# Kernel optimization log

Hardware: AMD Instinct MI355X
Metric: run time of the kernel (lower is better)

## Reference

```python
import jax, jax.numpy as jnp
import numpy as np

N_NODES = 100000
N_EDGES = 1000000
N_GRAPHS = 1024
F_IN = 128
N_CLASSES = 10
BN_EPS = 1e-5


def _lin(key, fan_in, fan_out):
    k1, k2 = jax.random.split(key)
    b = 1.0 / np.sqrt(fan_in)
    W = jax.random.uniform(k1, (fan_out, fan_in), minval=-b, maxval=b, dtype=jnp.float32)
    bias = jax.random.uniform(k2, (fan_out,), minval=-b, maxval=b, dtype=jnp.float32)
    return W, bias


def setup_inputs() -> dict:
    key = jax.random.key(0)
    ks = jax.random.split(key, 16)
    inp = {
        "atom_feats": jax.random.normal(ks[0], (N_NODES, F_IN), dtype=jnp.float32),
        "edge_src": jax.random.randint(ks[1], (N_EDGES,), 0, N_NODES),
        "edge_dst": jax.random.randint(ks[2], (N_EDGES,), 0, N_NODES),
        "graph_ids": jnp.sort(jax.random.randint(ks[3], (N_NODES,), 0, N_GRAPHS)),
    }
    # conv1: F_IN -> 32 with batch-norm on edge features
    inp["Wt1"], inp["bt1"] = _lin(ks[4], F_IN, 32)
    inp["Wp1"], inp["bp1"] = _lin(ks[5], F_IN, 32)
    inp["bn_gamma"] = jnp.ones((32,), jnp.float32)
    inp["bn_beta"] = jnp.zeros((32,), jnp.float32)
    inp["bn_mean"] = jnp.zeros((32,), jnp.float32)
    inp["bn_var"] = jnp.ones((32,), jnp.float32)
    # conv2: 32 -> 64 ; conv3: 64 -> 64
    inp["Wt2"], inp["bt2"] = _lin(ks[6], 32, 64)
    inp["Wp2"], inp["bp2"] = _lin(ks[7], 32, 64)
    inp["Wt3"], inp["bt3"] = _lin(ks[8], 64, 64)
    inp["Wp3"], inp["bp3"] = _lin(ks[9], 64, 64)
    # fc layers
    inp["Wf1"], inp["bf1"] = _lin(ks[10], 64, 64)
    inp["Wf2"], inp["bf2"] = _lin(ks[11], 64, 32)
    inp["Wf3"], inp["bf3"] = _lin(ks[12], 32, N_CLASSES)
    return inp


def _seg_max(vals, ids, n):
    m = jax.ops.segment_max(vals, ids, num_segments=n)
    return jnp.where(jnp.isfinite(m), m, 0.0)  # zero-in-degree -> 0 (DGL semantics)


def _edgeconv(x, src, dst, Wt, bt, Wp, bp, bn=None):
    xs = x[src]                      # [E, f_in] gather src
    xd = x[dst]                      # [E, f_in] gather dst
    e = (xd - xs) @ Wt.T + bt + (xs @ Wp.T + bp)  # [E, f_out]
    if bn is not None:
        gamma, beta, mean, var = bn
        e = (e - mean) * (gamma / jnp.sqrt(var + BN_EPS)) + beta
    return _seg_max(e, dst, x.shape[0])


def reference(atom_feats, edge_src, edge_dst, graph_ids,
              Wt1, bt1, Wp1, bp1, bn_gamma, bn_beta, bn_mean, bn_var,
              Wt2, bt2, Wp2, bp2, Wt3, bt3, Wp3, bp3,
              Wf1, bf1, Wf2, bf2, Wf3, bf3):
    x = jax.nn.elu(_edgeconv(atom_feats, edge_src, edge_dst, Wt1, bt1, Wp1, bp1,
                             bn=(bn_gamma, bn_beta, bn_mean, bn_var)))
    x = jax.nn.elu(_edgeconv(x, edge_src, edge_dst, Wt2, bt2, Wp2, bp2))
    x = jax.nn.elu(_edgeconv(x, edge_src, edge_dst, Wt3, bt3, Wp3, bp3))
    x = _seg_max(x, graph_ids, N_GRAPHS)          # graph-level max pooling [G, 64]
    x = jax.nn.elu(x @ Wf1.T + bf1)               # dropout is identity in eval mode
    x = jax.nn.elu(x @ Wf2.T + bf2)
    x = x @ Wf3.T + bf3
    return jax.nn.log_softmax(x, axis=1)
```

## Files before the change

kernel.cpp:

```cpp
#include <hip/hip_runtime.h>
#include <hip/hip_fp16.h>
#include <math.h>

#define N_NODES 100000
#define N_EDGES 1000000
#define N_GRAPHS 1024
#define BN_EPS 1e-5f

#define BUCKET_NODES 128
#define NB_BUCKETS ((N_NODES + BUCKET_NODES - 1) / BUCKET_NODES)
#define BUCKET_PAD 2048
#define BUCKET_CAP 3072
#define SCAT_CHUNK 2048

typedef __attribute__((__ext_vector_type__(8))) _Float16 f16x8;
typedef __attribute__((__ext_vector_type__(4))) _Float16 f16x4;
typedef __attribute__((__ext_vector_type__(4))) float f32x4;

static __device__ __forceinline__ float elu_f(float v) {
    return v > 0.f ? v : expm1f(v);
}

static __device__ __forceinline__ unsigned pkmax(unsigned a, unsigned b) {
    unsigned r;
    asm("v_pk_max_f16 %0, %1, %2" : "=v"(r) : "v"(a), "v"(b));
    return r;
}
#define HALF2_NEG_INF 0xFC00FC00u

static __device__ __forceinline__ uint4 pkmax4(uint4 a, uint4 b) {
    uint4 r;
    r.x = pkmax(a.x, b.x);
    r.y = pkmax(a.y, b.y);
    r.z = pkmax(a.z, b.z);
    r.w = pkmax(a.w, b.w);
    return r;
}

static __device__ __forceinline__ unsigned fmap(float f) {
    unsigned u = __float_as_uint(f);
    return (u & 0x80000000u) ? ~u : (u | 0x80000000u);
}
static __device__ __forceinline__ float funmap(unsigned u) {
    unsigned b = (u & 0x80000000u) ? (u & 0x7FFFFFFFu) : ~u;
    return __uint_as_float(b);
}
#define NEG_INF_MAPPED 0x007FFFFFu

__global__ __launch_bounds__(256) void prep_kernel(
        const float* __restrict__ Wt1, const float* __restrict__ bt1,
        const float* __restrict__ Wp1, const float* __restrict__ bp1,
        const float* __restrict__ gamma, const float* __restrict__ beta,
        const float* __restrict__ mean,  const float* __restrict__ var,
        const float* __restrict__ Wt2, const float* __restrict__ bt2,
        const float* __restrict__ Wp2, const float* __restrict__ bp2,
        const float* __restrict__ Wt3, const float* __restrict__ bt3,
        const float* __restrict__ Wp3, const float* __restrict__ bp3,
        __half* __restrict__ wsz1, float* __restrict__ qb1,
        __half* __restrict__ wsz2, float* __restrict__ qb2,
        __half* __restrict__ wsz3, float* __restrict__ qb3,
        int* __restrict__ cursor, unsigned* __restrict__ pooled) {
    int idx = blockIdx.x * 256 + threadIdx.x;

    if (idx < NB_BUCKETS) cursor[idx] = 0;
    for (int j = idx; j < N_GRAPHS * 64; j += 8192) pooled[j] = NEG_INF_MAPPED;

    {
        const int K = 128, F = 32, NCF = 4;
        if (idx < K * 2 * F) {
            int frag = idx >> 9, within = idx & 511, lane = within >> 3, j = within & 7;
            int kf = frag / NCF, cf = frag % NCF;
            int k = kf * 32 + (lane >> 4) * 8 + j;
            int c = cf * 16 + (lane & 15);
            float v;
            if (c < F) {
                float s = gamma[c] * rsqrtf(var[c] + BN_EPS);
                v = Wt1[c * K + k] * s;
            } else {
                int cc = c - F;
                float s = gamma[cc] * rsqrtf(var[cc] + BN_EPS);
                v = (Wp1[cc * K + k] - Wt1[cc * K + k]) * s;
            }
            wsz1[idx] = __float2half(v);
        }
        if (idx < F) {
            float s = gamma[idx] * rsqrtf(var[idx] + BN_EPS);
            qb1[idx] = (bt1[idx] + bp1[idx]) * s + beta[idx] - mean[idx] * s;
        }
    }
    {
        const int K = 32, F = 64, NCF = 8;
        if (idx < K * 2 * F) {
            int frag = idx >> 9, within = idx & 511, lane = within >> 3, j = within & 7;
            int kf = frag / NCF, cf = frag % NCF;
            int k = kf * 32 + (lane >> 4) * 8 + j;
            int c = cf * 16 + (lane & 15);
            float v = (c < F) ? Wt2[c * K + k]
                              : (Wp2[(c - F) * K + k] - Wt2[(c - F) * K + k]);
            wsz2[idx] = __float2half(v);
        }
        if (idx < F) qb2[idx] = bt2[idx] + bp2[idx];
    }
    {
        const int K = 64, F = 64, NCF = 8;
        if (idx < K * 2 * F) {
            int frag = idx >> 9, within = idx & 511, lane = within >> 3, j = within & 7;
            int kf = frag / NCF, cf = frag % NCF;
            int k = kf * 32 + (lane >> 4) * 8 + j;
            int c = cf * 16 + (lane & 15);
            float v = (c < F) ? Wt3[c * K + k]
                              : (Wp3[(c - F) * K + k] - Wt3[(c - F) * K + k]);
            wsz3[idx] = __float2half(v);
        }
        if (idx < F) qb3[idx] = bt3[idx] + bp3[idx];
    }
}

__global__ __launch_bounds__(256) void scatter_kernel(const int* __restrict__ esrc,
                                                      const int* __restrict__ edst,
                                                      int* __restrict__ cursor,
                                                      unsigned* __restrict__ binned, int E) {
    __shared__ int hist[NB_BUCKETS];
    __shared__ int lbase[NB_BUCKETS];
    __shared__ unsigned pk[SCAT_CHUNK];
    __shared__ unsigned short bk[SCAT_CHUNK];
    int begE = blockIdx.x * SCAT_CHUNK;
    int endE = min(begE + SCAT_CHUNK, E);
    int n = endE - begE;
    for (int i = threadIdx.x; i < NB_BUCKETS; i += 256) hist[i] = 0;
    __syncthreads();
    for (int i = threadIdx.x; i < n; i += 256) {
        int d = edst[begE + i];
        int s = esrc[begE + i];
        int b = d >> 7;
        pk[i] = ((unsigned)s << 7) | (unsigned)(d & 127);
        bk[i] = (unsigned short)b;
        atomicAdd(&hist[b], 1);
    }
    __syncthreads();
    for (int i = threadIdx.x; i < NB_BUCKETS; i += 256) {
        int c = hist[i];
        lbase[i] = c ? (i * BUCKET_PAD + atomicAdd(&cursor[i], c)) : 0;
        hist[i] = 0;
    }
    __syncthreads();
    for (int i = threadIdx.x; i < n; i += 256) {
        int b = bk[i];
        int pos = lbase[b] + atomicAdd(&hist[b], 1);
        binned[pos] = pk[i];
    }
}

__global__ __launch_bounds__(256) void bucket_build_kernel(const unsigned* __restrict__ binned,
                                                           const int* __restrict__ bcount,
                                                           int* __restrict__ begs,
                                                           int* __restrict__ ends,
                                                           int* __restrict__ csr) {
    __shared__ unsigned stage[BUCKET_CAP];
    __shared__ int srcLDS[BUCKET_CAP];
    __shared__ int cnt[BUCKET_NODES];
    __shared__ int sc[BUCKET_NODES];
    __shared__ int loff[BUCKET_NODES];

    int b = blockIdx.x;
    int ebeg = b * BUCKET_PAD;
    int ne = min(bcount[b], BUCKET_CAP);
    int tid = threadIdx.x;

    if (tid < BUCKET_NODES) cnt[tid] = 0;
    __syncthreads();
    for (int i = tid; i < ne; i += 256) {
        unsigned e = binned[ebeg + i];
        stage[i] = e;
        atomicAdd(&cnt[e & 127], 1);
    }
    __syncthreads();
    int v = (tid < BUCKET_NODES) ? cnt[tid] : 0;
    if (tid < BUCKET_NODES) sc[tid] = v;
    __syncthreads();
    for (int off = 1; off < BUCKET_NODES; off <<= 1) {
        int u = (tid < BUCKET_NODES && tid >= off) ? sc[tid - off] : 0;
        __syncthreads();
        if (tid < BUCKET_NODES) sc[tid] += u;
        __syncthreads();
    }
    if (tid < BUCKET_NODES) {
        loff[tid] = sc[tid] - v;
        cnt[tid] = 0;
    }
    __syncthreads();
    int gnode = b * BUCKET_NODES + tid;
    if (tid < BUCKET_NODES && gnode < N_NODES) {
        begs[gnode] = ebeg + loff[tid];
        ends[gnode] = ebeg + loff[tid] + v;
    }
    for (int i = tid; i < ne; i += 256) {
        unsigned e = stage[i];
        int ln = e & 127;
        int slot = loff[ln] + atomicAdd(&cnt[ln], 1);
        srcLDS[slot] = (int)(e >> 7);
    }
    __syncthreads();
    for (int i = tid; i < ne; i += 256) csr[ebeg + i] = srcLDS[i];
}

template <int K>
static __device__ __forceinline__ f16x8 load_afrag(const __half* __restrict__ x,
                                                   size_t rowIdx, int kOff) {
    return *reinterpret_cast<const f16x8*>(x + rowIdx * K + kOff);
}
template <int K>
static __device__ __forceinline__ f16x8 load_afrag(const float* __restrict__ x,
                                                   size_t rowIdx, int kOff) {
    const float* xr = x + rowIdx * K + kOff;
    float4 a0 = *reinterpret_cast<const float4*>(xr);
    float4 a1 = *reinterpret_cast<const float4*>(xr + 4);
    f16x8 a;
    a[0] = (_Float16)a0.x; a[1] = (_Float16)a0.y; a[2] = (_Float16)a0.z; a[3] = (_Float16)a0.w;
    a[4] = (_Float16)a1.x; a[5] = (_Float16)a1.y; a[6] = (_Float16)a1.z; a[7] = (_Float16)a1.w;
    return a;
}

template <int K, int F, typename IT>
__global__ __launch_bounds__(256) void transform_mfma(
        const IT* __restrict__ x, const __half* __restrict__ wsz,
        const float* __restrict__ qb,
        __half* __restrict__ t, __half* __restrict__ q) {
    constexpr int NKF = K / 32;
    constexpr int NCF = (2 * F) / 16;
    constexpr int NTILES = N_NODES / 16;

    int lane = threadIdx.x & 63;
    int wid = blockIdx.x * 4 + (threadIdx.x >> 6);
    int nWaves = gridDim.x * 4;

    f16x8 bfrag[NKF][NCF];
#pragma unroll
    for (int kf = 0; kf < NKF; kf++)
#pragma unroll
        for (int cf = 0; cf < NCF; cf++)
            bfrag[kf][cf] = *reinterpret_cast<const f16x8*>(
                wsz + ((size_t)(kf * NCF + cf) * 64 + lane) * 8);

    int row = lane & 15;
    int kq = lane >> 4;
    int col = lane & 15;
    int rbase = (lane >> 4) * 4;

    for (int tile = wid; tile < NTILES; tile += nWaves) {
        size_t nodeBase = (size_t)tile * 16;

        f32x4 acc[NCF];
#pragma unroll
        for (int cf = 0; cf < NCF; cf++) acc[cf] = (f32x4){0.f, 0.f, 0.f, 0.f};

#pragma unroll
        for (int kf = 0; kf < NKF; kf++) {
            f16x8 a = load_afrag<K>(x, nodeBase + row, kf * 32 + kq * 8);
#pragma unroll
            for (int cf = 0; cf < NCF; cf++)
                acc[cf] = __builtin_amdgcn_mfma_f32_16x16x32_f16(a, bfrag[kf][cf], acc[cf], 0, 0, 0);
        }

#pragma unroll
        for (int cf = 0; cf < NCF; cf++) {
            int c = cf * 16 + col;
            if (c < F) {
#pragma unroll
                for (int r = 0; r < 4; r++) {
                    size_t node = nodeBase + rbase + r;
                    t[node * F + c] = __float2half(acc[cf][r]);
                }
            } else {
                float qbv = qb[c - F];
#pragma unroll
                for (int r = 0; r < 4; r++) {
                    size_t node = nodeBase + rbase + r;
                    q[node * F + (c - F)] = __float2half(acc[cf][r] + qbv);
                }
            }
        }
    }
}

template <int F>
__global__ __launch_bounds__(256) void edgemax_kernel(
        const uint4* __restrict__ t16, const uint4* __restrict__ q16,
        const int* __restrict__ begs, const int* __restrict__ ends,
        const int* __restrict__ csr,
        uint4* __restrict__ out, int N) {
    constexpr int NPG = F / 8;
    constexpr int G = 256 / NPG;
    int g = threadIdx.x / NPG;
    int cp = threadIdx.x % NPG;
    int nd = blockIdx.x * G + g;
    if (nd >= N) return;
    int beg = begs[nd], end = ends[nd];

    uint4 mneg = {HALF2_NEG_INF, HALF2_NEG_INF, HALF2_NEG_INF, HALF2_NEG_INF};
    uint4 m0 = mneg, m1 = mneg;
    int i = beg;
    for (; i + 1 < end; i += 2) {
        int s0 = csr[i], s1 = csr[i + 1];
        uint4 v0 = q16[(size_t)s0 * NPG + cp];
        uint4 v1 = q16[(size_t)s1 * NPG + cp];
        m0 = pkmax4(m0, v0);
        m1 = pkmax4(m1, v1);
    }
    if (i < end) {
        m0 = pkmax4(m0, q16[(size_t)csr[i] * NPG + cp]);
    }
    uint4 m = pkmax4(m0, m1);

    uint4 res;
    if (beg < end) {
        uint4 tv = t16[(size_t)nd * NPG + cp];
        unsigned* mp = &m.x;
        unsigned* tp = &tv.x;
        unsigned* rp = &res.x;
#pragma unroll
        for (int w = 0; w < 4; w++) {
            float2 mf = __half22float2(__builtin_bit_cast(__half2, mp[w]));
            float2 tf = __half22float2(__builtin_bit_cast(__half2, tp[w]));
            float rx = elu_f(tf.x + mf.x);
            float ry = elu_f(tf.y + mf.y);
            rp[w] = __builtin_bit_cast(unsigned, __floats2half2_rn(rx, ry));
        }
    } else {
        res = (uint4){0u, 0u, 0u, 0u};
    }
    out[(size_t)nd * NPG + cp] = res;
}

__global__ void pool_kernel(const __half* __restrict__ x, const int* __restrict__ gid,
                            unsigned* __restrict__ pooled, int N) {
    const int CHUNK = 64;
    int wave = (blockIdx.x * blockDim.x + threadIdx.x) >> 6;
    int lane = threadIdx.x & 63;
    int start = wave * CHUNK;
    if (start >= N) return;
    int end = min(start + CHUNK, N);
    float m = -INFINITY;
    int cur = gid[start];
    for (int n = start; n < end; n++) {
        int g = gid[n];
        if (g != cur) {
            atomicMax(&pooled[cur * 64 + lane], fmap(m));
            cur = g;
            m = -INFINITY;
        }
        m = fmaxf(m, __half2float(x[(size_t)n * 64 + lane]));
    }
    atomicMax(&pooled[cur * 64 + lane], fmap(m));
}

__global__ __launch_bounds__(64) void fc_kernel(
        const unsigned* __restrict__ pooled,
        const float* __restrict__ Wf1, const float* __restrict__ bf1,
        const float* __restrict__ Wf2, const float* __restrict__ bf2,
        const float* __restrict__ Wf3, const float* __restrict__ bf3,
        float* __restrict__ out) {
    int g = blockIdx.x;
    int c = threadIdx.x;
    __shared__ float x0[64], h1[64], h2[32], h3[10];

    unsigned u = pooled[g * 64 + c];
    x0[c] = (u == NEG_INF_MAPPED) ? 0.f : funmap(u);
    __syncthreads();

    float a = bf1[c];
#pragma unroll 8
    for (int k = 0; k < 64; k++) a = fmaf(Wf1[c * 64 + k], x0[k], a);
    h1[c] = elu_f(a);
    __syncthreads();

    if (c < 32) {
        float a2 = bf2[c];
#pragma unroll 8
        for (int k = 0; k < 64; k++) a2 = fmaf(Wf2[c * 64 + k], h1[k], a2);
        h2[c] = elu_f(a2);
    }
    __syncthreads();

    if (c < 10) {
        float a3 = bf3[c];
#pragma unroll 8
        for (int k = 0; k < 32; k++) a3 = fmaf(Wf3[c * 32 + k], h2[k], a3);
        h3[c] = a3;
    }
    __syncthreads();

    if (c < 10) {
        float mx = h3[0];
#pragma unroll
        for (int j = 1; j < 10; j++) mx = fmaxf(mx, h3[j]);
        float s = 0.f;
#pragma unroll
        for (int j = 0; j < 10; j++) s += expf(h3[j] - mx);
        out[g * 10 + c] = h3[c] - mx - logf(s);
    }
}

extern "C" void kernel_launch(void* const* d_in, const int* in_sizes, int n_in,
                              void* d_out, int out_size, void* d_ws, size_t ws_size,
                              hipStream_t stream) {
    const float* atom = (const float*)d_in[0];
    const int* esrc = (const int*)d_in[1];
    const int* edst = (const int*)d_in[2];
    const int* gid  = (const int*)d_in[3];
    const float* Wt1 = (const float*)d_in[4];
    const float* bt1 = (const float*)d_in[5];
    const float* Wp1 = (const float*)d_in[6];
    const float* bp1 = (const float*)d_in[7];
    const float* bng = (const float*)d_in[8];
    const float* bnb = (const float*)d_in[9];
    const float* bnm = (const float*)d_in[10];
    const float* bnv = (const float*)d_in[11];
    const float* Wt2 = (const float*)d_in[12];
    const float* bt2 = (const float*)d_in[13];
    const float* Wp2 = (const float*)d_in[14];
    const float* bp2 = (const float*)d_in[15];
    const float* Wt3 = (const float*)d_in[16];
    const float* bt3 = (const float*)d_in[17];
    const float* Wp3 = (const float*)d_in[18];
    const float* bp3 = (const float*)d_in[19];
    const float* Wf1 = (const float*)d_in[20];
    const float* bf1 = (const float*)d_in[21];
    const float* Wf2 = (const float*)d_in[22];
    const float* bf2 = (const float*)d_in[23];
    const float* Wf3 = (const float*)d_in[24];
    const float* bf3 = (const float*)d_in[25];

    char* p = (char*)d_ws;
    auto alloc = [&](size_t bytes) -> void* {
        void* r = (void*)p;
        p += (bytes + 255) & ~(size_t)255;
        return r;
    };
    int* begs        = (int*)alloc(sizeof(int) * N_NODES);
    int* ends        = (int*)alloc(sizeof(int) * N_NODES);
    int* cursor      = (int*)alloc(sizeof(int) * NB_BUCKETS);
    unsigned* binned = (unsigned*)alloc(sizeof(unsigned) * NB_BUCKETS * BUCKET_PAD);
    int* csr         = (int*)alloc(sizeof(int) * NB_BUCKETS * BUCKET_PAD);
    __half* wsz1 = (__half*)alloc(sizeof(__half) * 128 * 64);
    __half* wsz2 = (__half*)alloc(sizeof(__half) * 32 * 128);
    __half* wsz3 = (__half*)alloc(sizeof(__half) * 64 * 128);
    float* qb1   = (float*)alloc(sizeof(float) * 32);
    float* qb2   = (float*)alloc(sizeof(float) * 64);
    float* qb3   = (float*)alloc(sizeof(float) * 64);
    __half* tbuf = (__half*)alloc(sizeof(__half) * (size_t)N_NODES * 64);
    __half* qbuf = (__half*)alloc(sizeof(__half) * (size_t)N_NODES * 64);
    __half* xh   = (__half*)alloc(sizeof(__half) * (size_t)N_NODES * 64);
    unsigned* pooled = (unsigned*)alloc(sizeof(unsigned) * N_GRAPHS * 64);

    prep_kernel<<<32, 256, 0, stream>>>(Wt1, bt1, Wp1, bp1, bng, bnb, bnm, bnv,
                                        Wt2, bt2, Wp2, bp2, Wt3, bt3, Wp3, bp3,
                                        wsz1, qb1, wsz2, qb2, wsz3, qb3, cursor, pooled);
    scatter_kernel<<<(N_EDGES + SCAT_CHUNK - 1) / SCAT_CHUNK, 256, 0, stream>>>(
        esrc, edst, cursor, binned, N_EDGES);
    bucket_build_kernel<<<NB_BUCKETS, 256, 0, stream>>>(binned, cursor, begs, ends, csr);

    transform_mfma<128, 32, float><<<1024, 256, 0, stream>>>(atom, wsz1, qb1, tbuf, qbuf);
    edgemax_kernel<32><<<(N_NODES + 63) / 64, 256, 0, stream>>>(
        (const uint4*)tbuf, (const uint4*)qbuf, begs, ends, csr, (uint4*)xh, N_NODES);

    transform_mfma<32, 64, __half><<<1024, 256, 0, stream>>>(xh, wsz2, qb2, tbuf, qbuf);
    edgemax_kernel<64><<<(N_NODES + 31) / 32, 256, 0, stream>>>(
        (const uint4*)tbuf, (const uint4*)qbuf, begs, ends, csr, (uint4*)xh, N_NODES);

    transform_mfma<64, 64, __half><<<1024, 256, 0, stream>>>(xh, wsz3, qb3, tbuf, qbuf);
    edgemax_kernel<64><<<(N_NODES + 31) / 32, 256, 0, stream>>>(
        (const uint4*)tbuf, (const uint4*)qbuf, begs, ends, csr, (uint4*)xh, N_NODES);

    {
        int waves = (N_NODES + 63) / 64;
        int blocks = (waves + 3) / 4;
        pool_kernel<<<blocks, 256, 0, stream>>>(xh, gid, pooled, N_NODES);
    }

    fc_kernel<<<N_GRAPHS, 64, 0, stream>>>(pooled, Wf1, bf1, Wf2, bf2, Wf3, bf3, (float*)d_out);
}
```

Baseline: 178.4 us.

## Store node features in 16-channel column-chunk layout and run edge-max per chunk

Node feature buffers become channel-blocked: each 16-channel chunk holds all nodes contiguously, so one chunk of the gather table is 3.2 MB in fp16. The edge-max kernel runs once per chunk (2 or 4 launches), so each pass gathers randomly from a smaller working set that fits better in cache. The transform and pool kernels index the new layout. The trade-offs are more launches, reading the CSR indices again in every pass, and 32-byte gather segments per edge instead of full 64/128-byte rows.

```diff
diff --git a/kernel.cpp b/kernel.cpp
--- a/kernel.cpp
+++ b/kernel.cpp
@@ -14,7 +14,6 @@
 #define SCAT_CHUNK 2048
 
 typedef __attribute__((__ext_vector_type__(8))) _Float16 f16x8;
-typedef __attribute__((__ext_vector_type__(4))) _Float16 f16x4;
 typedef __attribute__((__ext_vector_type__(4))) float f32x4;
 
 static __device__ __forceinline__ float elu_f(float v) {
@@ -206,13 +205,14 @@
 
 template <int K>
 static __device__ __forceinline__ f16x8 load_afrag(const __half* __restrict__ x,
-                                                   size_t rowIdx, int kOff) {
-    return *reinterpret_cast<const f16x8*>(x + rowIdx * K + kOff);
+                                                   size_t node, int kOff) {
+    return *reinterpret_cast<const f16x8*>(
+        x + ((size_t)(kOff >> 4) * N_NODES + node) * 16 + (kOff & 15));
 }
 template <int K>
 static __device__ __forceinline__ f16x8 load_afrag(const float* __restrict__ x,
-                                                   size_t rowIdx, int kOff) {
-    const float* xr = x + rowIdx * K + kOff;
+                                                   size_t node, int kOff) {
+    const float* xr = x + node * K + kOff;
     float4 a0 = *reinterpret_cast<const float4*>(xr);
     float4 a1 = *reinterpret_cast<const float4*>(xr + 4);
     f16x8 a;
@@ -269,31 +269,29 @@
 #pragma unroll
                 for (int r = 0; r < 4; r++) {
                     size_t node = nodeBase + rbase + r;
-                    t[node * F + c] = __float2half(acc[cf][r]);
+                    t[((size_t)(c >> 4) * N_NODES + node) * 16 + (c & 15)] = __float2half(acc[cf][r]);
                 }
             } else {
-                float qbv = qb[c - F];
+                int cc = c - F;
+                float qbv = qb[cc];
 #pragma unroll
                 for (int r = 0; r < 4; r++) {
                     size_t node = nodeBase + rbase + r;
-                    q[node * F + (c - F)] = __float2half(acc[cf][r] + qbv);
+                    q[((size_t)(cc >> 4) * N_NODES + node) * 16 + (cc & 15)] = __float2half(acc[cf][r] + qbv);
                 }
             }
         }
     }
 }
 
-template <int F>
-__global__ __launch_bounds__(256) void edgemax_kernel(
-        const uint4* __restrict__ t16, const uint4* __restrict__ q16,
+__global__ __launch_bounds__(256) void edgemax_pass_kernel(
+        const uint4* __restrict__ tc,
+        const uint4* __restrict__ qc,
         const int* __restrict__ begs, const int* __restrict__ ends,
         const int* __restrict__ csr,
-        uint4* __restrict__ out, int N) {
-    constexpr int NPG = F / 8;
-    constexpr int G = 256 / NPG;
-    int g = threadIdx.x / NPG;
-    int cp = threadIdx.x % NPG;
-    int nd = blockIdx.x * G + g;
+        uint4* __restrict__ outc, int N) {
+    int nd = blockIdx.x * 128 + (threadIdx.x >> 1);
+    int cp = threadIdx.x & 1;
     if (nd >= N) return;
     int beg = begs[nd], end = ends[nd];
 
@@ -301,20 +299,21 @@
     uint4 m0 = mneg, m1 = mneg;
     int i = beg;
     for (; i + 1 < end; i += 2) {
-        int s0 = csr[i], s1 = csr[i + 1];
-        uint4 v0 = q16[(size_t)s0 * NPG + cp];
-        uint4 v1 = q16[(size_t)s1 * NPG + cp];
+        int s0 = csr[i];
+        int s1 = csr[i + 1];
+        uint4 v0 = qc[(size_t)s0 * 2 + cp];
+        uint4 v1 = qc[(size_t)s1 * 2 + cp];
         m0 = pkmax4(m0, v0);
         m1 = pkmax4(m1, v1);
     }
     if (i < end) {
-        m0 = pkmax4(m0, q16[(size_t)csr[i] * NPG + cp]);
+        m0 = pkmax4(m0, qc[(size_t)csr[i] * 2 + cp]);
     }
     uint4 m = pkmax4(m0, m1);
 
     uint4 res;
     if (beg < end) {
-        uint4 tv = t16[(size_t)nd * NPG + cp];
+        uint4 tv = tc[(size_t)nd * 2 + cp];
         unsigned* mp = &m.x;
         unsigned* tp = &tv.x;
         unsigned* rp = &res.x;
@@ -329,7 +328,7 @@
     } else {
         res = (uint4){0u, 0u, 0u, 0u};
     }
-    out[(size_t)nd * NPG + cp] = res;
+    outc[(size_t)nd * 2 + cp] = res;
 }
 
 __global__ void pool_kernel(const __half* __restrict__ x, const int* __restrict__ gid,
@@ -340,6 +339,7 @@
     int start = wave * CHUNK;
     if (start >= N) return;
     int end = min(start + CHUNK, N);
+    const __half* base = x + (size_t)(lane >> 4) * N_NODES * 16 + (lane & 15);
     float m = -INFINITY;
     int cur = gid[start];
     for (int n = start; n < end; n++) {
@@ -349,7 +349,7 @@
             cur = g;
             m = -INFINITY;
         }
-        m = fmaxf(m, __half2float(x[(size_t)n * 64 + lane]));
+        m = fmaxf(m, __half2float(base[(size_t)n * 16]));
     }
     atomicMax(&pooled[cur * 64 + lane], fmap(m));
 }
@@ -453,6 +453,9 @@
     __half* xh   = (__half*)alloc(sizeof(__half) * (size_t)N_NODES * 64);
     unsigned* pooled = (unsigned*)alloc(sizeof(unsigned) * N_GRAPHS * 64);
 
+    const int NBLK = (N_NODES + 127) / 128;
+    const size_t CHW = (size_t)N_NODES * 16;
+
     prep_kernel<<<32, 256, 0, stream>>>(Wt1, bt1, Wp1, bp1, bng, bnb, bnm, bnv,
                                         Wt2, bt2, Wp2, bp2, Wt3, bt3, Wp3, bp3,
                                         wsz1, qb1, wsz2, qb2, wsz3, qb3, cursor, pooled);
@@ -461,16 +464,22 @@
     bucket_build_kernel<<<NB_BUCKETS, 256, 0, stream>>>(binned, cursor, begs, ends, csr);
 
     transform_mfma<128, 32, float><<<1024, 256, 0, stream>>>(atom, wsz1, qb1, tbuf, qbuf);
-    edgemax_kernel<32><<<(N_NODES + 63) / 64, 256, 0, stream>>>(
-        (const uint4*)tbuf, (const uint4*)qbuf, begs, ends, csr, (uint4*)xh, N_NODES);
+    for (int c = 0; c < 2; c++)
+        edgemax_pass_kernel<<<NBLK, 256, 0, stream>>>(
+            (const uint4*)(tbuf + c * CHW), (const uint4*)(qbuf + c * CHW),
+            begs, ends, csr, (uint4*)(xh + c * CHW), N_NODES);
 
     transform_mfma<32, 64, __half><<<1024, 256, 0, stream>>>(xh, wsz2, qb2, tbuf, qbuf);
-    edgemax_kernel<64><<<(N_NODES + 31) / 32, 256, 0, stream>>>(
-        (const uint4*)tbuf, (const uint4*)qbuf, begs, ends, csr, (uint4*)xh, N_NODES);
+    for (int c = 0; c < 4; c++)
+        edgemax_pass_kernel<<<NBLK, 256, 0, stream>>>(
+            (const uint4*)(tbuf + c * CHW), (const uint4*)(qbuf + c * CHW),
+            begs, ends, csr, (uint4*)(xh + c * CHW), N_NODES);
 
     transform_mfma<64, 64, __half><<<1024, 256, 0, stream>>>(xh, wsz3, qb3, tbuf, qbuf);
-    edgemax_kernel<64><<<(N_NODES + 31) / 32, 256, 0, stream>>>(
-        (const uint4*)tbuf, (const uint4*)qbuf, begs, ends, csr, (uint4*)xh, N_NODES);
+    for (int c = 0; c < 4; c++)
+        edgemax_pass_kernel<<<NBLK, 256, 0, stream>>>(
+            (const uint4*)(tbuf + c * CHW), (const uint4*)(qbuf + c * CHW),
+            begs, ends, csr, (uint4*)(xh + c * CHW), N_NODES);
 
     {
         int waves = (N_NODES + 63) / 64;
```

Result: slower. 242.8 us (+36.1%).
